# Performance work log

Measured on AMD Instinct MI355X. Metric: run time of the kernel, lower is better.

## Reference

```python
import jax, jax.numpy as jnp
import numpy as np

NUM_HEADS = 12
WS = 8
ROPE_BASE = 100.0  # croco/dust3r RoPE2D default frequency base


def _rope1d(t, p, inv_freq):
    # t: [Bw, h, N, d], p: [Bw, N], inv_freq: [d/2]
    freqs = p[..., None] * inv_freq                      # [Bw, N, d/2]
    emb = jnp.concatenate([freqs, freqs], axis=-1)       # [Bw, N, d]
    cos = jnp.cos(emb)[:, None, :, :]
    sin = jnp.sin(emb)[:, None, :, :]
    t1, t2 = jnp.split(t, 2, axis=-1)
    rot = jnp.concatenate([-t2, t1], axis=-1)            # rotate_half
    return t * cos + rot * sin


def _rope2d(tokens, pos):
    # tokens: [Bw, h, N, D], pos: [Bw, N, 2] (y, x). First D/2 dims use y, last D/2 use x.
    D = tokens.shape[-1]
    d = D // 2
    inv_freq = 1.0 / (ROPE_BASE ** (jnp.arange(0, d, 2, dtype=jnp.float32) / d))
    ty, tx = jnp.split(tokens, 2, axis=-1)
    return jnp.concatenate([_rope1d(ty, pos[..., 0], inv_freq),
                            _rope1d(tx, pos[..., 1], inv_freq)], axis=-1)


def setup_inputs() -> dict:
    B, H, W, C = 16, 64, 64, 768
    key = jax.random.key(0)
    ks = jax.random.split(key, 7)
    x_img = jax.random.normal(ks[0], (B, H * W, C), dtype=jnp.float32)
    yy, xx = jnp.meshgrid(jnp.arange(H), jnp.arange(W), indexing='ij')
    pos = jnp.stack([yy, xx], axis=-1).reshape(1, H * W, 2).astype(jnp.float32)
    pos2d_img = jnp.broadcast_to(pos, (B, H * W, 2))
    unseen = jax.random.normal(ks[1], (B, C), dtype=jnp.float32)
    sc = C ** -0.5
    qkv_w = jax.random.normal(ks[2], (3 * C, C), dtype=jnp.float32) * sc
    qkv_b = jax.random.normal(ks[3], (3 * C,), dtype=jnp.float32) * 0.02
    proj_w = jax.random.normal(ks[4], (C, C), dtype=jnp.float32) * sc
    proj_b = jax.random.normal(ks[5], (C,), dtype=jnp.float32) * 0.02
    return {'x_img': x_img, 'pos2d_img': pos2d_img, 'unseen': unseen,
            'qkv_w': qkv_w, 'qkv_b': qkv_b, 'proj_w': proj_w, 'proj_b': proj_b,
            'H': H, 'W': W}


def reference(x_img, pos2d_img, unseen, qkv_w, qkv_b, proj_w, proj_b, H, W):
    B, HW, C = x_img.shape
    hd = C // NUM_HEADS
    scale = hd ** -0.5
    nWh, nWw = H // WS, W // WS
    Bwin, Nwin = B * nWh * nWw, WS * WS

    # window partition
    xw = x_img.reshape(B, nWh, WS, nWw, WS, C).transpose(0, 1, 3, 2, 4, 5).reshape(Bwin, Nwin, C)
    pw = pos2d_img.reshape(B, nWh, WS, nWw, WS, 2).transpose(0, 1, 3, 2, 4, 5).reshape(Bwin, Nwin, 2)

    # append unseen token (shared across windows of an image)
    u = jnp.broadcast_to(unseen[:, None, None, :], (B, nWh * nWw, 1, C)).reshape(Bwin, 1, C)
    xw = jnp.concatenate([xw, u], axis=1)                # [Bwin, Nwin+1, C]

    qkv = xw @ qkv_w.T + qkv_b                           # [Bwin, N, 3C]
    qkv = qkv.reshape(Bwin, Nwin + 1, 3, NUM_HEADS, hd)
    q = qkv[:, :, 0].transpose(0, 2, 1, 3)               # [Bwin, h, N, hd]
    k = qkv[:, :, 1].transpose(0, 2, 1, 3)
    v = qkv[:, :, 2].transpose(0, 2, 1, 3)

    # RoPE2D on image tokens only; unseen token gets no RoPE
    q = jnp.concatenate([_rope2d(q[:, :, :Nwin], pw), q[:, :, Nwin:]], axis=2)
    k = jnp.concatenate([_rope2d(k[:, :, :Nwin], pw), k[:, :, Nwin:]], axis=2)

    attn = jax.nn.softmax(jnp.einsum('bhqd,bhkd->bhqk', q, k) * scale, axis=-1)
    out = jnp.einsum('bhqk,bhkd->bhqd', attn, v)
    out = out.transpose(0, 2, 1, 3).reshape(Bwin, Nwin + 1, C)
    out = out @ proj_w.T + proj_b

    # window merge
    out_img = out[:, :Nwin].reshape(B, nWh, nWw, WS, WS, C).transpose(0, 1, 3, 2, 4, 5).reshape(B, HW, C)
    out_unseen = out[:, Nwin].reshape(B, nWh * nWw, C).mean(axis=1)  # [B, C]
    return out_img, out_unseen
```

## Files before the change

kernel.cpp:

```cpp
#include <hip/hip_runtime.h>
#include <cstdint>
#include <cstddef>

typedef __attribute__((ext_vector_type(8)))  __bf16 bf16x8;
typedef __attribute__((ext_vector_type(4)))  float  f32x4;
typedef __attribute__((ext_vector_type(2)))  unsigned int u32x2;

#define DI __device__ __forceinline__

constexpr int Cdim = 768;
constexpr int C3   = 2304;
constexpr int NT   = 65;
constexpr int ROWS = 1024 * NT;
constexpr int ROWS_PAD = ROWS + 32;
constexpr int TP   = 96;
constexpr int PS   = 128;
constexpr long long OUT_IMG = 16LL * 4096 * 768;

DI float bf2f(unsigned short u) { unsigned int x = (unsigned int)u << 16; float f; __builtin_memcpy(&f, &x, 4); return f; }
DI unsigned short f2bf(float f) { unsigned int x; __builtin_memcpy(&x, &f, 4); x = x + 0x7fffu + ((x >> 16) & 1u); return (unsigned short)(x >> 16); }

DI void gload_lds16(const unsigned short* g, unsigned short* l) {
  __builtin_amdgcn_global_load_lds((__attribute__((address_space(1))) void*)g,
                                   (__attribute__((address_space(3))) void*)l, 16, 0, 0);
}

__global__ void k_prep(const float* __restrict__ qkv_w, const float* __restrict__ proj_w,
                       unsigned short* __restrict__ wqb, unsigned short* __restrict__ wpb,
                       float* __restrict__ rope) {
  const int NW1 = 2304 * 768;
  const int NW2 = 768 * 768;
  int total = NW1 + NW2 + 1024;
  for (int i = blockIdx.x * blockDim.x + threadIdx.x; i < total; i += gridDim.x * blockDim.x) {
    if (i < NW1) wqb[i] = f2bf(qkv_w[i]);
    else if (i < NW1 + NW2) wpb[i - NW1] = f2bf(proj_w[i - NW1]);
    else {
      int e = i - NW1 - NW2;
      int p = e >> 4, j = e & 15;
      float inv = powf(100.f, -(float)j * (1.f / 16.f));
      float a = (float)p * inv;
      rope[2 * e]     = cosf(a);
      rope[2 * e + 1] = sinf(a);
    }
  }
}

__global__ void k_xw(const float* __restrict__ x, const float* __restrict__ unseen,
                     unsigned short* __restrict__ xw) {
  int row = blockIdx.x;
  int w = row / NT, t = row - w * NT;
  const float* src;
  if (t == 64) {
    src = unseen + (size_t)(w >> 6) * Cdim;
  } else {
    int wy = (w >> 3) & 7, wx = w & 7;
    int hw = ((wy << 3) + (t >> 3)) * 64 + (wx << 3) + (t & 7);
    src = x + ((size_t)(w >> 6) * 4096 + hw) * Cdim;
  }
  float4 v = ((const float4*)src)[threadIdx.x];
  unsigned int u0 = (unsigned)f2bf(v.x) | ((unsigned)f2bf(v.y) << 16);
  unsigned int u1 = (unsigned)f2bf(v.z) | ((unsigned)f2bf(v.w) << 16);
  ((u32x2*)(xw + (size_t)row * Cdim))[threadIdx.x] = (u32x2){u0, u1};
}

template<int MODE, int NTILES>
__global__ __launch_bounds__(256, 2) void k_gemm(
    const unsigned short* __restrict__ A, const unsigned short* __restrict__ Bw,
    const float* __restrict__ bias, const float* __restrict__ rope,
    unsigned short* __restrict__ Cb, float* __restrict__ outp) {
  constexpr int K = 768;
  constexpr int NK = K / 64;
  __shared__ alignas(16) unsigned short As[256 * 64];
  __shared__ alignas(16) unsigned short Bs[128 * 64];

  constexpr int nwg = 260 * NTILES;
  constexpr int q8 = nwg / 8, r8 = nwg % 8;
  int id = blockIdx.x;
  int xcd = id & 7, lid = id >> 3;
  int wg = (xcd < r8 ? xcd * (q8 + 1) : r8 * (q8 + 1) + (xcd - r8) * q8) + lid;
  int mtile = wg / NTILES, ntile = wg - mtile * NTILES;
  int m0 = mtile * 256, n0 = ntile * 128;

  int tid = threadIdx.x;
  int lane = tid & 63, wid = tid >> 6;
  int lq = lane & 15, lg = lane >> 4;
  int wm = (wid >> 1) * 128;
  int wn = (wid & 1) * 64;

  f32x4 acc[8][4];
  #pragma unroll
  for (int i = 0; i < 8; ++i)
    #pragma unroll
    for (int j = 0; j < 4; ++j) acc[i][j] = (f32x4){0.f, 0.f, 0.f, 0.f};

  #pragma unroll 1
  for (int kt = 0; kt < NK; ++kt) {
    int k0 = kt * 64;
    #pragma unroll
    for (int j = 0; j < 8; ++j) {
      int slot = j * 256 + tid;
      int row = slot >> 3, c = slot & 7;
      gload_lds16(A + (size_t)(m0 + row) * K + k0 + (c ^ (row & 7)) * 8,
                  As + (size_t)(j * 256 + (tid & ~63)) * 8);
    }
    #pragma unroll
    for (int j = 0; j < 4; ++j) {
      int slot = j * 256 + tid;
      int row = slot >> 3, c = slot & 7;
      gload_lds16(Bw + (size_t)(n0 + row) * K + k0 + (c ^ (row & 7)) * 8,
                  Bs + (size_t)(j * 256 + (tid & ~63)) * 8);
    }
    __syncthreads();

    bf16x8 bfr[8];
    #pragma unroll
    for (int nf = 0; nf < 4; ++nf)
      #pragma unroll
      for (int ks = 0; ks < 2; ++ks) {
        int row = wn + nf * 16 + lq;
        bfr[nf * 2 + ks] = *(const bf16x8*)(Bs + row * 64 + (((ks * 4 + lg) ^ (row & 7)) * 8));
      }
    #pragma unroll
    for (int half = 0; half < 2; ++half) {
      bf16x8 af[8];
      #pragma unroll
      for (int mf = 0; mf < 4; ++mf)
        #pragma unroll
        for (int ks = 0; ks < 2; ++ks) {
          int row = wm + half * 64 + mf * 16 + lq;
          af[mf * 2 + ks] = *(const bf16x8*)(As + row * 64 + (((ks * 4 + lg) ^ (row & 7)) * 8));
        }
      #pragma unroll
      for (int mf = 0; mf < 4; ++mf)
        #pragma unroll
        for (int nf = 0; nf < 4; ++nf)
          #pragma unroll
          for (int ks = 0; ks < 2; ++ks)
            acc[half * 4 + mf][nf] =
              __builtin_amdgcn_mfma_f32_16x16x32_bf16(af[mf * 2 + ks], bfr[nf * 2 + ks],
                                                      acc[half * 4 + mf][nf], 0, 0, 0);
    }
    __syncthreads();
  }

  #pragma unroll
  for (int mf = 0; mf < 8; ++mf) {
    #pragma unroll
    for (int r = 0; r < 4; ++r) {
      int row = m0 + wm + mf * 16 + (lg << 2) + r;
      int w = row / NT, t = row - w * NT;
      int wy = (w >> 3) & 7, wx = w & 7;
      int py = (wy << 3) + (t >> 3), px = (wx << 3) + (t & 7);
      #pragma unroll
      for (int a = 0; a < 2; ++a) {
        int col0 = n0 + wn + a * 32 + lq;
        int col1 = col0 + 16;
        float v0 = acc[mf][2 * a][r] + bias[col0];
        float v1 = acc[mf][2 * a + 1][r] + bias[col1];
        if (MODE == 0) {
          if (col0 < 1536 && t != 64) {
            int p = a ? px : py;
            const float* rp = rope + ((p << 4) + lq) * 2;
            float cc = rp[0], ss = rp[1];
            float o0 = v0 * cc - v1 * ss;
            float o1 = v1 * cc + v0 * ss;
            v0 = o0; v1 = o1;
          }
          unsigned short* cr = Cb + (size_t)row * C3;
          cr[col0] = f2bf(v0);
          cr[col1] = f2bf(v1);
        } else {
          if (t == 64) {
            float* ub = outp + OUT_IMG + (size_t)(w >> 6) * Cdim;
            atomicAdd(ub + col0, v0 * (1.f / 64.f));
            atomicAdd(ub + col1, v1 * (1.f / 64.f));
          } else {
            float* orow = outp + ((size_t)(w >> 6) * 4096 + py * 64 + px) * Cdim;
            orow[col0] = v0;
            orow[col1] = v1;
          }
        }
      }
    }
  }
}

__global__ void k_vt(const unsigned short* __restrict__ qkv, unsigned short* __restrict__ Vt) {
  int bh = blockIdx.x;
  int w = bh / 12, h = bh - w * 12;
  __shared__ float sv[65][65];
  const unsigned short* base = qkv + (size_t)w * NT * C3 + 1536 + h * 64;
  for (int i = threadIdx.x; i < 65 * 64; i += 256) {
    int t = i >> 6, d = i & 63;
    sv[t][d] = bf2f(base[(size_t)t * C3 + d]);
  }
  __syncthreads();
  unsigned short* out = Vt + (size_t)bh * 64 * TP;
  for (int i = threadIdx.x; i < 64 * TP; i += 256) {
    int d = i / TP, t = i - d * TP;
    out[i] = f2bf(t < 65 ? sv[t][d] : 0.f);
  }
}

__global__ __launch_bounds__(64) void k_attn(const unsigned short* __restrict__ qkv,
                                             const unsigned short* __restrict__ Vt,
                                             unsigned short* __restrict__ att) {
  __shared__ alignas(16) unsigned short P[80 * PS];
  int h = blockIdx.x, w = blockIdx.y;
  int lane = threadIdx.x;
  int lq = lane & 15, lg = lane >> 4;

  const unsigned short* qb = qkv + (size_t)w * NT * C3 + h * 64;
  const unsigned short* kb = qb + 768;

  bf16x8 kf[5][2];
  #pragma unroll
  for (int kt = 0; kt < 5; ++kt)
    #pragma unroll
    for (int ks = 0; ks < 2; ++ks)
      kf[kt][ks] = *(const bf16x8*)(kb + (size_t)(kt * 16 + lq) * C3 + ks * 32 + lg * 8);

  const unsigned short* vb = Vt + (size_t)(w * 12 + h) * 64 * TP;
  bf16x8 vf[3][4];
  #pragma unroll
  for (int ks = 0; ks < 3; ++ks)
    #pragma unroll
    for (int dt = 0; dt < 4; ++dt)
      vf[ks][dt] = *(const bf16x8*)(vb + (size_t)(dt * 16 + lq) * TP + ks * 32 + lg * 8);

  for (int i = lane; i < 80 * 8; i += 64) {
    int row = i >> 3, j = i & 7;
    int byteo = row * (PS * 2) + 160 + j * 4;
    byteo ^= (row & 7) << 4;
    *(unsigned int*)((char*)P + byteo) = 0u;
  }

  #pragma unroll 1
  for (int qt = 0; qt < 5; ++qt) {
    bf16x8 qf[2];
    #pragma unroll
    for (int ks = 0; ks < 2; ++ks)
      qf[ks] = *(const bf16x8*)(qb + (size_t)(qt * 16 + lq) * C3 + ks * 32 + lg * 8);

    f32x4 sa[5];
    #pragma unroll
    for (int kt = 0; kt < 5; ++kt) {
      sa[kt] = (f32x4){0.f, 0.f, 0.f, 0.f};
      #pragma unroll
      for (int ks = 0; ks < 2; ++ks)
        sa[kt] = __builtin_amdgcn_mfma_f32_16x16x32_bf16(kf[kt][ks], qf[ks], sa[kt], 0, 0, 0);
    }
    float pv[5][4];
    float m = -1e30f;
    #pragma unroll
    for (int kt = 0; kt < 5; ++kt)
      #pragma unroll
      for (int r = 0; r < 4; ++r) {
        int tok = kt * 16 + lg * 4 + r;
        float s = sa[kt][r] * 0.125f;
        bool ok = tok < 65;
        pv[kt][r] = ok ? s : -1e30f;
        m = (ok && s > m) ? s : m;
      }
    m = fmaxf(m, __shfl_xor(m, 16));
    m = fmaxf(m, __shfl_xor(m, 32));
    float sum = 0.f;
    #pragma unroll
    for (int kt = 0; kt < 5; ++kt)
      #pragma unroll
      for (int r = 0; r < 4; ++r) {
        float e = (pv[kt][r] > -1e29f) ? exp2f((pv[kt][r] - m) * 1.44269504f) : 0.f;
        pv[kt][r] = e;
        sum += e;
      }
    sum += __shfl_xor(sum, 16);
    sum += __shfl_xor(sum, 32);
    float rinv = 1.f / sum;

    int q = qt * 16 + lq;
    #pragma unroll
    for (int kt = 0; kt < 5; ++kt) {
      unsigned int u0 = (unsigned)f2bf(pv[kt][0] * rinv) | ((unsigned)f2bf(pv[kt][1] * rinv) << 16);
      unsigned int u1 = (unsigned)f2bf(pv[kt][2] * rinv) | ((unsigned)f2bf(pv[kt][3] * rinv) << 16);
      int byteo = q * (PS * 2) + kt * 32 + lg * 8;
      byteo ^= (q & 7) << 4;
      *(u32x2*)((char*)P + byteo) = (u32x2){u0, u1};
    }
    asm volatile("s_waitcnt lgkmcnt(0)" ::: "memory");

    bf16x8 bp[3];
    #pragma unroll
    for (int ks = 0; ks < 3; ++ks) {
      int byteo = q * (PS * 2) + ks * 64 + lg * 16;
      byteo ^= (q & 7) << 4;
      bp[ks] = *(const bf16x8*)((char*)P + byteo);
    }
    #pragma unroll
    for (int dt = 0; dt < 4; ++dt) {
      f32x4 o = (f32x4){0.f, 0.f, 0.f, 0.f};
      #pragma unroll
      for (int ks = 0; ks < 3; ++ks)
        o = __builtin_amdgcn_mfma_f32_16x16x32_bf16(vf[ks][dt], bp[ks], o, 0, 0, 0);
      if (q < 65) {
        unsigned int u0 = (unsigned)f2bf(o[0]) | ((unsigned)f2bf(o[1]) << 16);
        unsigned int u1 = (unsigned)f2bf(o[2]) | ((unsigned)f2bf(o[3]) << 16);
        *(u32x2*)(att + (size_t)(w * NT + q) * Cdim + h * 64 + dt * 16 + lg * 4) = (u32x2){u0, u1};
      }
    }
  }
}

extern "C" void kernel_launch(void* const* d_in, const int* in_sizes, int n_in,
                              void* d_out, int out_size, void* d_ws, size_t ws_size,
                              hipStream_t stream) {
  const float* x_img  = (const float*)d_in[0];
  const float* unseen = (const float*)d_in[2];
  const float* qkv_w  = (const float*)d_in[3];
  const float* qkv_b  = (const float*)d_in[4];
  const float* proj_w = (const float*)d_in[5];
  const float* proj_b = (const float*)d_in[6];

  char* ws = (char*)d_ws;
  size_t off = 0;
  auto alloc = [&](size_t bytes) { void* p = ws + off; off = (off + bytes + 255) & ~(size_t)255; return p; };
  unsigned short* xw  = (unsigned short*)alloc((size_t)ROWS * Cdim * 2);
  unsigned short* qkv = (unsigned short*)alloc((size_t)ROWS_PAD * C3 * 2);
  unsigned short* Vt  = (unsigned short*)alloc((size_t)12288 * 64 * TP * 2);
  unsigned short* wqb = (unsigned short*)alloc((size_t)C3 * Cdim * 2);
  unsigned short* wpb = (unsigned short*)alloc((size_t)Cdim * Cdim * 2);
  float* rope = (float*)alloc(64 * 16 * 2 * sizeof(float));

  hipMemsetAsync((float*)d_out + OUT_IMG, 0, 16 * Cdim * sizeof(float), stream);

  k_prep<<<512, 256, 0, stream>>>(qkv_w, proj_w, wqb, wpb, rope);
  k_xw<<<ROWS, 192, 0, stream>>>(x_img, unseen, xw);
  k_gemm<0, 18><<<260 * 18, 256, 0, stream>>>(xw, wqb, qkv_b, rope, qkv, nullptr);
  k_vt<<<12288, 256, 0, stream>>>(qkv, Vt);
  k_attn<<<dim3(12, 1024), 64, 0, stream>>>(qkv, Vt, xw);
  k_gemm<1, 6><<<260 * 6, 256, 0, stream>>>(xw, wpb, proj_b, nullptr, nullptr, (float*)d_out);
}
```

Baseline: 725.3 us.

## Fuse V transpose into QKV GEMM epilogue and double-buffer GEMM A tiles

The QKV GEMM epilogue now writes V directly in transposed per-head layout (64x64, no padding), which removes the separate k_vt kernel and its extra pass over V. Attention handles the 65th unseen key as a scalar FMA term instead of a padded third MFMA step, and the zero-fill of P is dropped. The GEMM main loop double-buffers the A tile in LDS and loads B fragments straight from global memory into registers, overlapping loads with compute. The costs are scattered 2-byte stores for V in the epilogue and higher register pressure from holding two sets of B fragments.

```diff
diff --git a/kernel.cpp b/kernel.cpp
--- a/kernel.cpp
+++ b/kernel.cpp
@@ -13,7 +13,6 @@
 constexpr int NT   = 65;
 constexpr int ROWS = 1024 * NT;
 constexpr int ROWS_PAD = ROWS + 32;
-constexpr int TP   = 96;
 constexpr int PS   = 128;
 constexpr long long OUT_IMG = 16LL * 4096 * 768;
 
@@ -67,11 +66,11 @@
 __global__ __launch_bounds__(256, 2) void k_gemm(
     const unsigned short* __restrict__ A, const unsigned short* __restrict__ Bw,
     const float* __restrict__ bias, const float* __restrict__ rope,
-    unsigned short* __restrict__ Cb, float* __restrict__ outp) {
+    unsigned short* __restrict__ Cb, unsigned short* __restrict__ Vt,
+    float* __restrict__ outp) {
   constexpr int K = 768;
-  constexpr int NK = K / 64;
-  __shared__ alignas(16) unsigned short As[256 * 64];
-  __shared__ alignas(16) unsigned short Bs[128 * 64];
+  constexpr int NK = 12;
+  __shared__ alignas(16) unsigned short As[2][256 * 64];
 
   constexpr int nwg = 260 * NTILES;
   constexpr int q8 = nwg / 8, r8 = nwg % 8;
@@ -87,39 +86,33 @@
   int wm = (wid >> 1) * 128;
   int wn = (wid & 1) * 64;
 
-  f32x4 acc[8][4];
-  #pragma unroll
-  for (int i = 0; i < 8; ++i)
-    #pragma unroll
-    for (int j = 0; j < 4; ++j) acc[i][j] = (f32x4){0.f, 0.f, 0.f, 0.f};
-
-  #pragma unroll 1
-  for (int kt = 0; kt < NK; ++kt) {
+  auto stageA = [&](int kt, int b) {
+    unsigned short* d = As[b];
     int k0 = kt * 64;
     #pragma unroll
     for (int j = 0; j < 8; ++j) {
       int slot = j * 256 + tid;
       int row = slot >> 3, c = slot & 7;
       gload_lds16(A + (size_t)(m0 + row) * K + k0 + (c ^ (row & 7)) * 8,
-                  As + (size_t)(j * 256 + (tid & ~63)) * 8);
-    }
-    #pragma unroll
-    for (int j = 0; j < 4; ++j) {
-      int slot = j * 256 + tid;
-      int row = slot >> 3, c = slot & 7;
-      gload_lds16(Bw + (size_t)(n0 + row) * K + k0 + (c ^ (row & 7)) * 8,
-                  Bs + (size_t)(j * 256 + (tid & ~63)) * 8);
-    }
-    __syncthreads();
-
-    bf16x8 bfr[8];
+                  d + (size_t)(j * 256 + (tid & ~63)) * 8);
+    }
+  };
+  auto loadB = [&](int kt, bf16x8* dst) {
+    const unsigned short* bp = Bw + (size_t)(n0 + wn + lq) * K + kt * 64 + lg * 8;
     #pragma unroll
     for (int nf = 0; nf < 4; ++nf)
       #pragma unroll
-      for (int ks = 0; ks < 2; ++ks) {
-        int row = wn + nf * 16 + lq;
-        bfr[nf * 2 + ks] = *(const bf16x8*)(Bs + row * 64 + (((ks * 4 + lg) ^ (row & 7)) * 8));
-      }
+      for (int ks = 0; ks < 2; ++ks)
+        dst[nf * 2 + ks] = *(const bf16x8*)(bp + (size_t)nf * 16 * K + ks * 32);
+  };
+
+  f32x4 acc[8][4];
+  #pragma unroll
+  for (int i = 0; i < 8; ++i)
+    #pragma unroll
+    for (int j = 0; j < 4; ++j) acc[i][j] = (f32x4){0.f, 0.f, 0.f, 0.f};
+
+  auto compute = [&](int b, bf16x8* bf) {
     #pragma unroll
     for (int half = 0; half < 2; ++half) {
       bf16x8 af[8];
@@ -128,7 +121,7 @@
         #pragma unroll
         for (int ks = 0; ks < 2; ++ks) {
           int row = wm + half * 64 + mf * 16 + lq;
-          af[mf * 2 + ks] = *(const bf16x8*)(As + row * 64 + (((ks * 4 + lg) ^ (row & 7)) * 8));
+          af[mf * 2 + ks] = *(const bf16x8*)(As[b] + row * 64 + (((ks * 4 + lg) ^ (row & 7)) * 8));
         }
       #pragma unroll
       for (int mf = 0; mf < 4; ++mf)
@@ -137,10 +130,25 @@
           #pragma unroll
           for (int ks = 0; ks < 2; ++ks)
             acc[half * 4 + mf][nf] =
-              __builtin_amdgcn_mfma_f32_16x16x32_bf16(af[mf * 2 + ks], bfr[nf * 2 + ks],
+              __builtin_amdgcn_mfma_f32_16x16x32_bf16(af[mf * 2 + ks], bf[nf * 2 + ks],
                                                       acc[half * 4 + mf][nf], 0, 0, 0);
     }
+  };
+
+  bf16x8 bA[8], bB[8];
+  stageA(0, 0);
+  loadB(0, bA);
+  __syncthreads();
+
+  #pragma unroll 1
+  for (int t = 0; t < NK; t += 2) {
+    stageA(t + 1, 1);
+    loadB(t + 1, bB);
+    compute(0, bA);
     __syncthreads();
+    if (t + 2 < NK) { stageA(t + 2, 0); loadB(t + 2, bA); }
+    compute(1, bB);
+    if (t + 2 < NK) __syncthreads();
   }
 
   #pragma unroll
@@ -158,17 +166,28 @@
         float v0 = acc[mf][2 * a][r] + bias[col0];
         float v1 = acc[mf][2 * a + 1][r] + bias[col1];
         if (MODE == 0) {
-          if (col0 < 1536 && t != 64) {
-            int p = a ? px : py;
-            const float* rp = rope + ((p << 4) + lq) * 2;
-            float cc = rp[0], ss = rp[1];
-            float o0 = v0 * cc - v1 * ss;
-            float o1 = v1 * cc + v0 * ss;
-            v0 = o0; v1 = o1;
+          unsigned short* cr = Cb + (size_t)row * C3;
+          if (col0 < 1536) {
+            if (t != 64) {
+              int p = a ? px : py;
+              const float* rp = rope + ((p << 4) + lq) * 2;
+              float cc = rp[0], ss = rp[1];
+              float o0 = v0 * cc - v1 * ss;
+              float o1 = v1 * cc + v0 * ss;
+              v0 = o0; v1 = o1;
+            }
+            cr[col0] = f2bf(v0);
+            cr[col1] = f2bf(v1);
+          } else if (t != 64) {
+            int c0 = col0 - 1536;
+            int h = c0 >> 6, d0 = c0 & 63;
+            unsigned short* vtb = Vt + (((size_t)w * 12 + h) << 12);
+            vtb[d0 * 64 + t] = f2bf(v0);
+            vtb[(d0 + 16) * 64 + t] = f2bf(v1);
+          } else {
+            cr[col0] = f2bf(v0);
+            cr[col1] = f2bf(v1);
           }
-          unsigned short* cr = Cb + (size_t)row * C3;
-          cr[col0] = f2bf(v0);
-          cr[col1] = f2bf(v1);
         } else {
           if (t == 64) {
             float* ub = outp + OUT_IMG + (size_t)(w >> 6) * Cdim;
@@ -185,23 +204,6 @@
   }
 }
 
-__global__ void k_vt(const unsigned short* __restrict__ qkv, unsigned short* __restrict__ Vt) {
-  int bh = blockIdx.x;
-  int w = bh / 12, h = bh - w * 12;
-  __shared__ float sv[65][65];
-  const unsigned short* base = qkv + (size_t)w * NT * C3 + 1536 + h * 64;
-  for (int i = threadIdx.x; i < 65 * 64; i += 256) {
-    int t = i >> 6, d = i & 63;
-    sv[t][d] = bf2f(base[(size_t)t * C3 + d]);
-  }
-  __syncthreads();
-  unsigned short* out = Vt + (size_t)bh * 64 * TP;
-  for (int i = threadIdx.x; i < 64 * TP; i += 256) {
-    int d = i / TP, t = i - d * TP;
-    out[i] = f2bf(t < 65 ? sv[t][d] : 0.f);
-  }
-}
-
 __global__ __launch_bounds__(64) void k_attn(const unsigned short* __restrict__ qkv,
                                              const unsigned short* __restrict__ Vt,
                                              unsigned short* __restrict__ att) {
@@ -220,19 +222,23 @@
     for (int ks = 0; ks < 2; ++ks)
       kf[kt][ks] = *(const bf16x8*)(kb + (size_t)(kt * 16 + lq) * C3 + ks * 32 + lg * 8);
 
-  const unsigned short* vb = Vt + (size_t)(w * 12 + h) * 64 * TP;
-  bf16x8 vf[3][4];
-  #pragma unroll
-  for (int ks = 0; ks < 3; ++ks)
+  const unsigned short* vb = Vt + (((size_t)w * 12 + h) << 12);
+  bf16x8 vf[2][4];
+  #pragma unroll
+  for (int ks = 0; ks < 2; ++ks)
     #pragma unroll
     for (int dt = 0; dt < 4; ++dt)
-      vf[ks][dt] = *(const bf16x8*)(vb + (size_t)(dt * 16 + lq) * TP + ks * 32 + lg * 8);
-
-  for (int i = lane; i < 80 * 8; i += 64) {
-    int row = i >> 3, j = i & 7;
-    int byteo = row * (PS * 2) + 160 + j * 4;
-    byteo ^= (row & 7) << 4;
-    *(unsigned int*)((char*)P + byteo) = 0u;
+      vf[ks][dt] = *(const bf16x8*)(vb + (size_t)(dt * 16 + lq) * 64 + ks * 32 + lg * 8);
+
+  const unsigned short* v64p = qb + 64 * C3 + 1536;
+  float v64f[4][4];
+  #pragma unroll
+  for (int dt = 0; dt < 4; ++dt) {
+    u32x2 u = *(const u32x2*)(v64p + dt * 16 + lg * 4);
+    v64f[dt][0] = bf2f((unsigned short)(u[0] & 0xffff));
+    v64f[dt][1] = bf2f((unsigned short)(u[0] >> 16));
+    v64f[dt][2] = bf2f((unsigned short)(u[1] & 0xffff));
+    v64f[dt][3] = bf2f((unsigned short)(u[1] >> 16));
   }
 
   #pragma unroll 1
@@ -279,18 +285,20 @@
 
     int q = qt * 16 + lq;
     #pragma unroll
-    for (int kt = 0; kt < 5; ++kt) {
+    for (int kt = 0; kt < 4; ++kt) {
       unsigned int u0 = (unsigned)f2bf(pv[kt][0] * rinv) | ((unsigned)f2bf(pv[kt][1] * rinv) << 16);
       unsigned int u1 = (unsigned)f2bf(pv[kt][2] * rinv) | ((unsigned)f2bf(pv[kt][3] * rinv) << 16);
       int byteo = q * (PS * 2) + kt * 32 + lg * 8;
       byteo ^= (q & 7) << 4;
       *(u32x2*)((char*)P + byteo) = (u32x2){u0, u1};
     }
+    float p64 = pv[4][0] * rinv;
+    p64 = __shfl(p64, lq);
     asm volatile("s_waitcnt lgkmcnt(0)" ::: "memory");
 
-    bf16x8 bp[3];
-    #pragma unroll
-    for (int ks = 0; ks < 3; ++ks) {
+    bf16x8 bp[2];
+    #pragma unroll
+    for (int ks = 0; ks < 2; ++ks) {
       int byteo = q * (PS * 2) + ks * 64 + lg * 16;
       byteo ^= (q & 7) << 4;
       bp[ks] = *(const bf16x8*)((char*)P + byteo);
@@ -299,8 +307,10 @@
     for (int dt = 0; dt < 4; ++dt) {
       f32x4 o = (f32x4){0.f, 0.f, 0.f, 0.f};
       #pragma unroll
-      for (int ks = 0; ks < 3; ++ks)
+      for (int ks = 0; ks < 2; ++ks)
         o = __builtin_amdgcn_mfma_f32_16x16x32_bf16(vf[ks][dt], bp[ks], o, 0, 0, 0);
+      #pragma unroll
+      for (int r = 0; r < 4; ++r) o[r] += p64 * v64f[dt][r];
       if (q < 65) {
         unsigned int u0 = (unsigned)f2bf(o[0]) | ((unsigned)f2bf(o[1]) << 16);
         unsigned int u1 = (unsigned)f2bf(o[2]) | ((unsigned)f2bf(o[3]) << 16);
@@ -325,7 +335,7 @@
   auto alloc = [&](size_t bytes) { void* p = ws + off; off = (off + bytes + 255) & ~(size_t)255; return p; };
   unsigned short* xw  = (unsigned short*)alloc((size_t)ROWS * Cdim * 2);
   unsigned short* qkv = (unsigned short*)alloc((size_t)ROWS_PAD * C3 * 2);
-  unsigned short* Vt  = (unsigned short*)alloc((size_t)12288 * 64 * TP * 2);
+  unsigned short* Vt  = (unsigned short*)alloc((size_t)12288 * 64 * 64 * 2);
   unsigned short* wqb = (unsigned short*)alloc((size_t)C3 * Cdim * 2);
   unsigned short* wpb = (unsigned short*)alloc((size_t)Cdim * Cdim * 2);
   float* rope = (float*)alloc(64 * 16 * 2 * sizeof(float));
@@ -334,8 +344,7 @@
 
   k_prep<<<512, 256, 0, stream>>>(qkv_w, proj_w, wqb, wpb, rope);
   k_xw<<<ROWS, 192, 0, stream>>>(x_img, unseen, xw);
-  k_gemm<0, 18><<<260 * 18, 256, 0, stream>>>(xw, wqb, qkv_b, rope, qkv, nullptr);
-  k_vt<<<12288, 256, 0, stream>>>(qkv, Vt);
+  k_gemm<0, 18><<<260 * 18, 256, 0, stream>>>(xw, wqb, qkv_b, rope, qkv, Vt, nullptr);
   k_attn<<<dim3(12, 1024), 64, 0, stream>>>(qkv, Vt, xw);
-  k_gemm<1, 6><<<260 * 6, 256, 0, stream>>>(xw, wpb, proj_b, nullptr, nullptr, (float*)d_out);
-}
+  k_gemm<1, 6><<<260 * 6, 256, 0, stream>>>(xw, wpb, proj_b, nullptr, nullptr, nullptr, (float*)d_out);
+}
```

Result: slower. 846.2 us (+16.7%).
